# Performance work log

Hardware: AMD Instinct MI355X
Metric: run time of the kernel (lower is better)

Reference implementation:

```python
import jax, jax.numpy as jnp
import numpy as np
from jax import lax

G = 8      # deform groups (weight groups == offset groups)
K = 3      # kernel size
K2 = K * K


def conv3x3(x, w, b):
    # NCHW, 3x3, stride 1, padding 1 (SAME)
    y = lax.conv_general_dilated(x, w, (1, 1), 'SAME',
                                 dimension_numbers=('NCHW', 'OIHW', 'NCHW'))
    return y + b[None, :, None, None]


def deform_conv2d(ref, offsets, w, b):
    # ref: [B,C,H,W], offsets: [B,2*G*K2,H,W] (torchvision layout: per group,
    # per kernel position, (dy, dx) pairs), w: [C_out, C_in/G, K, K], b: [C_out]
    B, C, H, W = ref.shape
    Cg = C // G
    off = offsets.reshape(B, G, K2, 2, H, W)
    dy = off[:, :, :, 0]  # [B,G,K2,H,W]
    dx = off[:, :, :, 1]
    ky = (jnp.arange(K2) // K - K // 2).astype(ref.dtype)  # kernel y offsets (pad=1)
    kx = (jnp.arange(K2) % K - K // 2).astype(ref.dtype)
    base_y = jnp.arange(H, dtype=ref.dtype)[:, None] + ky[:, None, None]  # [K2,H,1]
    base_x = jnp.arange(W, dtype=ref.dtype)[None, :] + kx[:, None, None]  # [K2,1,W]
    py = dy + base_y  # [B,G,K2,H,W]
    px = dx + base_x

    y0 = jnp.floor(py).astype(jnp.int32)
    x0 = jnp.floor(px).astype(jnp.int32)
    ly = py - y0.astype(ref.dtype)
    lx = px - x0.astype(ref.dtype)

    ref_flat = ref.reshape(B, G, Cg, H * W)

    def gather(yi, xi):
        valid = (yi >= 0) & (yi < H) & (xi >= 0) & (xi < W)
        idx = jnp.clip(yi, 0, H - 1) * W + jnp.clip(xi, 0, W - 1)  # [B,G,K2,H,W]
        vals = jnp.take_along_axis(ref_flat, idx.reshape(B, G, 1, K2 * H * W), axis=3)
        vals = vals.reshape(B, G, Cg, K2, H, W)
        return vals * valid[:, :, None].astype(ref.dtype)

    w00 = ((1 - ly) * (1 - lx))[:, :, None]
    w01 = ((1 - ly) * lx)[:, :, None]
    w10 = (ly * (1 - lx))[:, :, None]
    w11 = (ly * lx)[:, :, None]
    sampled = (w00 * gather(y0, x0) + w01 * gather(y0, x0 + 1)
               + w10 * gather(y0 + 1, x0) + w11 * gather(y0 + 1, x0 + 1))
    # grouped accumulation: weight [C_out, Cg, K, K] -> [G, OCg, Cg, K2]
    wg = w.reshape(G, C // G, Cg, K2)
    out = jnp.einsum('bgikhw,goik->bgohw', sampled, wg)
    return out.reshape(B, C, H, W) + b[None, :, None, None]


def setup_inputs() -> dict:
    key = jax.random.key(0)
    ks = jax.random.split(key, 10)
    B, C, H, W = 2, 64, 256, 256
    s64 = 1.0 / np.sqrt(C * 9)
    s128 = 1.0 / np.sqrt(128 * 9)
    return {
        'offset': jax.random.normal(ks[0], (B, C, H, W), jnp.float32),
        'ref': jax.random.normal(ks[1], (B, C, H, W), jnp.float32),
        'w_off': jax.random.normal(ks[2], (2 * K2 * G, C, K, K), jnp.float32) * s64,
        'b_off': jnp.zeros((2 * K2 * G,), jnp.float32),
        'w_def': jax.random.normal(ks[3], (C, C // G, K, K), jnp.float32) * (1.0 / np.sqrt((C // G) * 9)),
        'b_def': jnp.zeros((C,), jnp.float32),
        'w_r1': jax.random.normal(ks[4], (C, 2 * C, K, K), jnp.float32) * s128,
        'b_r1': jnp.zeros((C,), jnp.float32),
        'w_r2': jax.random.normal(ks[5], (C, C, K, K), jnp.float32) * s64,
        'b_r2': jnp.zeros((C,), jnp.float32),
    }


def reference(offset, ref, w_off, b_off, w_def, b_def, w_r1, b_r1, w_r2, b_r2):
    deform_offsets = conv3x3(offset, w_off, b_off)              # [B,144,H,W]
    aligned_ref = deform_conv2d(ref, deform_offsets, w_def, b_def)
    x = jnp.concatenate([ref, aligned_ref], axis=1)             # [B,128,H,W]
    x = jax.nn.relu(conv3x3(x, w_r1, b_r1))
    x = jax.nn.relu(conv3x3(x, w_r2, b_r2))
    return x + aligned_ref
```

## Files before the change

### kernel.cpp

```cpp
#include <hip/hip_runtime.h>

typedef __attribute__((ext_vector_type(8)))  short  short8;
typedef __attribute__((ext_vector_type(4)))  float  float4v;
typedef __attribute__((ext_vector_type(16))) float  float16v;
typedef __attribute__((ext_vector_type(2)))  float  f32x2;

constexpr int HH = 256, WW = 256;
constexpr int PD = 258;
constexpr int PR = 260;
constexpr size_t HWsz = (size_t)HH * WW;

__device__ inline unsigned short f2bf(float f) {
    unsigned int u = __builtin_bit_cast(unsigned int, f);
    u += 0x7FFFu + ((u >> 16) & 1u);
    return (unsigned short)(u >> 16);
}
__device__ inline float bfhalf(unsigned int w, int hi) {
    return __builtin_bit_cast(float, hi ? (w & 0xFFFF0000u) : (w << 16));
}
__device__ inline f32x2 unpk2(unsigned int w) {
    f32x2 r;
    r.x = __builtin_bit_cast(float, w << 16);
    r.y = __builtin_bit_cast(float, w & 0xFFFF0000u);
    return r;
}
__device__ inline f32x2 splat2(float s) { f32x2 r; r.x = s; r.y = s; return r; }

template<int CDST, bool WRITE_G>
__global__ __launch_bounds__(256) void nchw_to_nhwc(
    const float* __restrict__ src, unsigned short* __restrict__ dst,
    unsigned short* __restrict__ dst_g)
{
    const int px = threadIdx.x, h = blockIdx.x, bi = blockIdx.y;
    const float* s = src + (size_t)bi * 64 * HWsz + (size_t)h * WW + px;
    unsigned short* d = dst + (((size_t)bi * PD + (h + 1)) * PD + (px + 1)) * CDST;
#pragma unroll
    for (int cg = 0; cg < 8; ++cg) {
        float v[8];
#pragma unroll
        for (int j = 0; j < 8; ++j) v[j] = s[(size_t)(cg * 8 + j) * HWsz];
        uint4 pk;
        pk.x = f2bf(v[0]) | ((unsigned)f2bf(v[1]) << 16);
        pk.y = f2bf(v[2]) | ((unsigned)f2bf(v[3]) << 16);
        pk.z = f2bf(v[4]) | ((unsigned)f2bf(v[5]) << 16);
        pk.w = f2bf(v[6]) | ((unsigned)f2bf(v[7]) << 16);
        *(uint4*)&d[cg * 8] = pk;
        if (WRITE_G) {
            unsigned short* dg = dst_g +
                ((size_t)(bi * 8 + cg) * PR * PR + (size_t)(h + 1) * PR + (px + 1)) * 8;
            *(uint4*)dg = pk;
        }
    }
}

__global__ __launch_bounds__(256) void zero_border(
    unsigned short* __restrict__ p_off, unsigned short* __restrict__ p_cat,
    unsigned short* __restrict__ p_x1, unsigned short* __restrict__ refg)
{
    const int bi = blockIdx.y, which = blockIdx.z;
    if (which == 3) {
        const int total = 8 * 1548;
        for (int i = blockIdx.x * 256 + threadIdx.x; i < total; i += gridDim.x * 256) {
            int g = i / 1548, t = i - g * 1548;
            int r, c;
            if (t < 780)  { int rr = t / 260; c = t - rr * 260; r = rr == 0 ? 0 : 256 + rr; }
            else          { int u = t - 780; int cc = u >> 8; r = 1 + (u & 255); c = cc == 0 ? 0 : 256 + cc; }
            uint4 z = {0, 0, 0, 0};
            *(uint4*)&refg[((size_t)(bi * 8 + g) * PR * PR + (size_t)r * PR + c) * 8] = z;
        }
        return;
    }
    unsigned short* buf = which == 0 ? p_off : (which == 1 ? p_cat : p_x1);
    const int CIN = (which == 1) ? 128 : 64;
    const int NG = CIN / 8;
    unsigned short* p = buf + (size_t)bi * PD * PD * CIN;
    const int total = 1028 * 16;
    for (int i = blockIdx.x * 256 + threadIdx.x; i < total; i += gridDim.x * 256) {
        int g = i & 15;
        if (g >= NG) continue;
        int pxi = i >> 4;
        int r, c;
        if (pxi < 258)       { r = 0;   c = pxi; }
        else if (pxi < 516)  { r = 257; c = pxi - 258; }
        else if (pxi < 772)  { r = pxi - 516 + 1; c = 0; }
        else                 { r = pxi - 772 + 1; c = 257; }
        uint4 z = {0, 0, 0, 0};
        *(uint4*)&p[((size_t)r * PD + c) * CIN + g * 8] = z;
    }
}

__device__ inline void pack_one(const float* __restrict__ w, short* __restrict__ wpk,
                                int Cout, int Cin, int e)
{
    int j = e & 7;
    int lane = (e >> 3) & 63;
    int ksp = 9 * (Cin / 16);
    int kstep = (e >> 9) % ksp;
    int cot = (e >> 9) / ksp;
    int tap = kstep / (Cin / 16);
    int ci = (kstep % (Cin / 16)) * 16 + (lane >> 5) * 8 + j;
    int co = cot * 32 + (lane & 31);
    float v = (co < Cout) ? w[((size_t)co * Cin + ci) * 9 + tap] : 0.f;
    wpk[e] = (short)f2bf(v);
}

__global__ __launch_bounds__(256) void pack_all(
    const float* __restrict__ w1, short* __restrict__ d1,
    const float* __restrict__ w2, short* __restrict__ d2,
    const float* __restrict__ w3, short* __restrict__ d3)
{
    int e = blockIdx.x * 256 + threadIdx.x;
    if (e < 110592)               pack_one(w1, d1, 144, 64, e);
    else if (e < 110592 + 73728)  pack_one(w2, d2, 64, 128, e - 110592);
    else if (e < 221184)          pack_one(w3, d3, 64, 64,  e - 184320);
}

template<int CIN, int COF, int COTB, int MODE, int MINW>
__global__ __launch_bounds__(256, MINW) void conv_mfma_nb(
    const unsigned short* __restrict__ src,
    const short* __restrict__ wpk,
    const float* __restrict__ bias,
    unsigned short* __restrict__ dst_bf,
    float* __restrict__ dst_f,
    const unsigned short* __restrict__ resid_bf)
{
    constexpr int CHUNKS = CIN / 32;
    constexpr int KST = 9 * (CIN / 16);
    constexpr int WSEG = 3 * 4 * 66 * 8;

    __shared__ unsigned short lds[4 * WSEG];

    const int tid  = threadIdx.x;
    const int lane = tid & 63;
    const int wv   = tid >> 6;
    const int half = lane >> 5;
    const int n32  = lane & 31;
    const int h  = blockIdx.x;
    const int bi = blockIdx.y / COTB;
    const int cb = blockIdx.y % COTB;
    const int cbase = cb * COF * 32;

    unsigned short* my = lds + wv * WSEG;
    const unsigned short* srcB = src + (size_t)bi * PD * PD * CIN;
    const short8* wbase = (const short8*)wpk;

    float16v acc[COF][2];
#pragma unroll
    for (int f = 0; f < COF; ++f) {
        float16v bv;
#pragma unroll
        for (int reg = 0; reg < 16; ++reg) {
            int co = cbase + f * 32 + (reg >> 2) * 8 + 4 * half + (reg & 3);
            float b = 0.f;
            if (MODE != 0 || co < 144) b = bias[co];
            bv[reg] = b;
        }
        acc[f][0] = bv;
        acc[f][1] = bv;
    }

    for (int ch = 0; ch < CHUNKS; ++ch) {
        const unsigned short* gband = srcB + ((size_t)h * PD + wv * 64) * CIN + ch * 32;
#pragma unroll
        for (int i0 = 0; i0 < 264; i0 += 64) {
            int i = i0 + lane;
            if (i0 + 64 > 264 && i >= 264) continue;
            int px = i >> 2, o = i & 3;
#pragma unroll
            for (int r = 0; r < 3; ++r) {
                uint4 v = *(const uint4*)(gband + ((size_t)r * PD + px) * CIN + o * 8);
                *(uint4*)&my[(((size_t)r * 4 + o) * 66 + px) * 8] = v;
            }
        }

#pragma unroll
        for (int tap = 0; tap < 9; ++tap) {
            const int row = tap / 3, dxo = tap % 3;
#pragma unroll
            for (int s = 0; s < 2; ++s) {
                const int kstep = tap * (CIN / 16) + ch * 2 + s;
                short8 a[COF];
#pragma unroll
                for (int f = 0; f < COF; ++f)
                    a[f] = wbase[((size_t)(cb * COF + f) * KST + kstep) * 64 + lane];
#pragma unroll
                for (int nt = 0; nt < 2; ++nt) {
                    short8 b = *(const short8*)
                        &my[(((size_t)row * 4 + s * 2 + half) * 66 + nt * 32 + dxo + n32) * 8];
#pragma unroll
                    for (int f = 0; f < COF; ++f)
                        acc[f][nt] = __builtin_amdgcn_mfma_f32_32x32x16_bf16(a[f], b, acc[f][nt], 0, 0, 0);
                }
            }
        }
    }

#pragma unroll
    for (int f = 0; f < COF; ++f) {
#pragma unroll
        for (int nt = 0; nt < 2; ++nt) {
            const int px = wv * 64 + nt * 32 + n32;
            float16v a = acc[f][nt];
#pragma unroll
            for (int q = 0; q < 4; ++q) {
                const int co4 = cbase + f * 32 + q * 8 + 4 * half;
                float v0 = a[q * 4 + 0], v1 = a[q * 4 + 1];
                float v2 = a[q * 4 + 2], v3 = a[q * 4 + 3];
                if (MODE == 0) {
                    if (co4 < 144) {
                        unsigned short* d = dst_bf + (size_t)bi * HWsz * 144;
                        uint2 pk;
                        pk.x = f2bf(v0) | ((unsigned)f2bf(v1) << 16);
                        pk.y = f2bf(v2) | ((unsigned)f2bf(v3) << 16);
                        *(uint2*)&d[((size_t)h * WW + px) * 144 + co4] = pk;
                    }
                } else if (MODE == 1) {
                    unsigned short* d = dst_bf + (size_t)bi * PD * PD * 64;
                    uint2 pk;
                    pk.x = f2bf(fmaxf(v0, 0.f)) | ((unsigned)f2bf(fmaxf(v1, 0.f)) << 16);
                    pk.y = f2bf(fmaxf(v2, 0.f)) | ((unsigned)f2bf(fmaxf(v3, 0.f)) << 16);
                    *(uint2*)&d[(((size_t)h + 1) * PD + (px + 1)) * 64 + co4] = pk;
                } else {
                    const unsigned short* rp = resid_bf + (size_t)bi * PD * PD * 128;
                    uint2 rv = *(const uint2*)&rp[(((size_t)h + 1) * PD + (px + 1)) * 128 + 64 + co4];
                    float r0 = bfhalf(rv.x, 0), r1 = bfhalf(rv.x, 1);
                    float r2 = bfhalf(rv.y, 0), r3 = bfhalf(rv.y, 1);
                    float* d = dst_f + (size_t)bi * 64 * HWsz + (size_t)h * WW + px;
                    d[(size_t)(co4 + 0) * HWsz] = fmaxf(v0, 0.f) + r0;
                    d[(size_t)(co4 + 1) * HWsz] = fmaxf(v1, 0.f) + r1;
                    d[(size_t)(co4 + 2) * HWsz] = fmaxf(v2, 0.f) + r2;
                    d[(size_t)(co4 + 3) * HWsz] = fmaxf(v3, 0.f) + r3;
                }
            }
        }
    }
}

__global__ __launch_bounds__(256) void deform_k7(
    const unsigned short* __restrict__ refg,
    const unsigned short* __restrict__ doff,
    const float* __restrict__ wdef, const float* __restrict__ bdef,
    unsigned short* __restrict__ pcat_out)
{
    __shared__ float wsm2[576];
    const int L = blockIdx.x;
    const int xcd = L & 7;
    const int j = L >> 3;
    const int g = j & 7;
    const int r = (j >> 3) & 31;
    const int bi = j >> 8;
    const int h = xcd * 32 + r;
    const int px = threadIdx.x;

    for (int i = threadIdx.x; i < 576; i += 256) {
        int o = i & 7, c = (i >> 3) & 7, k = i >> 6;
        wsm2[i] = wdef[(size_t)g * 576 + o * 72 + c * 9 + k];
    }
    __syncthreads();

    const unsigned int* dp = (const unsigned int*)(
        doff + (((size_t)bi * HWsz) + (size_t)h * WW + px) * 144 + g * 18);
    unsigned int dw[9];
#pragma unroll
    for (int k = 0; k < 9; ++k) dw[k] = dp[k];

    f32x2 acc2[4];
#pragma unroll
    for (int o = 0; o < 4; ++o) {
        acc2[o].x = bdef[g * 8 + 2 * o];
        acc2[o].y = bdef[g * 8 + 2 * o + 1];
    }

    const unsigned short* rb = refg + (size_t)(bi * 8 + g) * PR * PR * 8;
    const float hf = (float)h, pxf = (float)px;

#pragma unroll
    for (int k = 0; k < 9; ++k) {
        float dy = bfhalf(dw[k], 0);
        float dx = bfhalf(dw[k], 1);
        float py  = dy + (hf + (float)(k / 3 - 1));
        float pxs = dx + (pxf + (float)(k % 3 - 1));
        py  = fminf(fmaxf(py,  -1.f), 256.f);
        pxs = fminf(fmaxf(pxs, -1.f), 256.f);
        float fy = floorf(py), fx = floorf(pxs);
        float ly = py - fy, lx = pxs - fx;
        int y0 = (int)fy, x0 = (int)fx;
        int i00 = (y0 + 1) * PR + (x0 + 1);
        float omly = 1.f - ly, omlx = 1.f - lx;
        f32x2 w00 = splat2(omly * omlx), w01 = splat2(omly * lx);
        f32x2 w10 = splat2(ly * omlx),  w11 = splat2(ly * lx);

        const uint4 q00 = *(const uint4*)(rb + (size_t)i00 * 8);
        const uint4 q01 = *(const uint4*)(rb + (size_t)(i00 + 1) * 8);
        const uint4 q10 = *(const uint4*)(rb + (size_t)(i00 + PR) * 8);
        const uint4 q11 = *(const uint4*)(rb + (size_t)(i00 + PR + 1) * 8);
        union U { uint4 v; unsigned int a[4]; };
        U u00{q00}, u01{q01}, u10{q10}, u11{q11};

#pragma unroll
        for (int cw = 0; cw < 4; ++cw) {
            f32x2 sv = unpk2(u00.a[cw]) * w00;
            sv = __builtin_elementwise_fma(unpk2(u01.a[cw]), w01, sv);
            sv = __builtin_elementwise_fma(unpk2(u10.a[cw]), w10, sv);
            sv = __builtin_elementwise_fma(unpk2(u11.a[cw]), w11, sv);
            f32x2 bx = splat2(sv.x);
            f32x2 by = splat2(sv.y);
            const f32x2* wpa = (const f32x2*)&wsm2[((k * 8) + cw * 2) * 8];
            const f32x2* wpb = (const f32x2*)&wsm2[((k * 8) + cw * 2 + 1) * 8];
#pragma unroll
            for (int o = 0; o < 4; ++o) {
                acc2[o] = __builtin_elementwise_fma(wpa[o], bx, acc2[o]);
                acc2[o] = __builtin_elementwise_fma(wpb[o], by, acc2[o]);
            }
        }
    }

    unsigned short* po = pcat_out + (((size_t)bi * PD + (h + 1)) * PD + (px + 1)) * 128 + 64 + g * 8;
    uint4 pk;
    pk.x = f2bf(acc2[0].x) | ((unsigned)f2bf(acc2[0].y) << 16);
    pk.y = f2bf(acc2[1].x) | ((unsigned)f2bf(acc2[1].y) << 16);
    pk.z = f2bf(acc2[2].x) | ((unsigned)f2bf(acc2[2].y) << 16);
    pk.w = f2bf(acc2[3].x) | ((unsigned)f2bf(acc2[3].y) << 16);
    *(uint4*)po = pk;
}

extern "C" void kernel_launch(void* const* d_in, const int* in_sizes, int n_in,
                              void* d_out, int out_size, void* d_ws, size_t ws_size,
                              hipStream_t stream)
{
    const float* offset = (const float*)d_in[0];
    const float* ref    = (const float*)d_in[1];
    const float* w_off  = (const float*)d_in[2];
    const float* b_off  = (const float*)d_in[3];
    const float* w_def  = (const float*)d_in[4];
    const float* b_def  = (const float*)d_in[5];
    const float* w_r1   = (const float*)d_in[6];
    const float* b_r1   = (const float*)d_in[7];
    const float* w_r2   = (const float*)d_in[8];
    const float* b_r2   = (const float*)d_in[9];
    float* out = (float*)d_out;

    unsigned short* p_off = (unsigned short*)d_ws;
    unsigned short* p_cat = p_off + (size_t)8520192;
    unsigned short* p_x1  = p_cat + (size_t)17040384;
    unsigned short* doff  = p_x1 + (size_t)8520192;
    unsigned short* refg  = doff + (size_t)18874368;
    short* wpk1  = (short*)(refg + (size_t)8652800);
    short* wpkr1 = wpk1 + 110592;
    short* wpkr2 = wpkr1 + 73728;

    zero_border<<<dim3(65, 2, 4), 256, 0, stream>>>(p_off, p_cat, p_x1, refg);

    pack_all<<<dim3((221184 + 255) / 256), 256, 0, stream>>>(
        w_off, wpk1, w_r1, wpkr1, w_r2, wpkr2);

    nchw_to_nhwc<64, false><<<dim3(256, 2), 256, 0, stream>>>(offset, p_off, nullptr);
    nchw_to_nhwc<128, true><<<dim3(256, 2), 256, 0, stream>>>(ref, p_cat, refg);

    conv_mfma_nb<64, 2, 3, 0, 3><<<dim3(256, 6), 256, 0, stream>>>(
        p_off, wpk1, b_off, doff, nullptr, nullptr);

    deform_k7<<<dim3(4096), 256, 0, stream>>>(refg, doff, w_def, b_def, p_cat);

    conv_mfma_nb<128, 2, 1, 1, 3><<<dim3(256, 2), 256, 0, stream>>>(
        p_cat, wpkr1, b_r1, p_x1, nullptr, nullptr);

    conv_mfma_nb<64, 2, 1, 2, 3><<<dim3(256, 2), 256, 0, stream>>>(
        p_x1, wpkr2, b_r2, nullptr, out, p_cat);
}
```

Before: 336.4 us.

## Double-buffer deform gathers and read prepacked weights from global instead of LDS

The deformable conv kernel now issues the four bilinear gathers for the next tap before doing the arithmetic for the current tap, using two register buffers to hide gather latency. The deform weights are repacked once in pack_all into a per-group float layout in workspace, so the kernel reads them through uniform global loads. This removes the per-block LDS fill and __syncthreads. A launch bound of 6 blocks per SM is also added. The extra live registers for the second buffer may limit occupancy, and scalar or global weight reads may be slower than LDS broadcast.

Result: slower. 478.0 us (+42.1%).

```diff
diff --git a/kernel.cpp b/kernel.cpp
--- a/kernel.cpp
+++ b/kernel.cpp
@@ -107,12 +107,19 @@
 __global__ __launch_bounds__(256) void pack_all(
     const float* __restrict__ w1, short* __restrict__ d1,
     const float* __restrict__ w2, short* __restrict__ d2,
-    const float* __restrict__ w3, short* __restrict__ d3)
+    const float* __restrict__ w3, short* __restrict__ d3,
+    const float* __restrict__ wdef, float* __restrict__ wdefp)
 {
     int e = blockIdx.x * 256 + threadIdx.x;
     if (e < 110592)               pack_one(w1, d1, 144, 64, e);
     else if (e < 110592 + 73728)  pack_one(w2, d2, 64, 128, e - 110592);
     else if (e < 221184)          pack_one(w3, d3, 64, 64,  e - 184320);
+    else if (e < 221184 + 4608) {
+        int t = e - 221184;
+        int o = t & 7, c = (t >> 3) & 7, gk = t >> 6;
+        int g = gk / 9, k = gk - g * 9;
+        wdefp[t] = wdef[(size_t)g * 576 + o * 72 + c * 9 + k];
+    }
 }
 
 template<int CIN, int COF, int COTB, int MODE, int MINW>
@@ -236,13 +243,63 @@
     }
 }
 
-__global__ __launch_bounds__(256) void deform_k7(
+__device__ __forceinline__ void tap_setup(int k, const unsigned int* dw,
+    float hf, float pxf, int& i00, float& ly, float& lx)
+{
+    float dy = bfhalf(dw[k], 0);
+    float dx = bfhalf(dw[k], 1);
+    float py  = dy + (hf + (float)(k / 3 - 1));
+    float pxs = dx + (pxf + (float)(k % 3 - 1));
+    py  = fminf(fmaxf(py,  -1.f), 256.f);
+    pxs = fminf(fmaxf(pxs, -1.f), 256.f);
+    float fy = floorf(py), fx = floorf(pxs);
+    ly = py - fy; lx = pxs - fx;
+    i00 = ((int)fy + 1) * PR + ((int)fx + 1);
+}
+
+__device__ __forceinline__ void tap_load(const unsigned short* __restrict__ rb,
+                                         int i00, uint4* q)
+{
+    q[0] = *(const uint4*)(rb + (size_t)(unsigned)i00 * 8);
+    q[1] = *(const uint4*)(rb + (size_t)(unsigned)(i00 + 1) * 8);
+    q[2] = *(const uint4*)(rb + (size_t)(unsigned)(i00 + PR) * 8);
+    q[3] = *(const uint4*)(rb + (size_t)(unsigned)(i00 + PR + 1) * 8);
+}
+
+__device__ __forceinline__ void tap_consume(const uint4* q, float ly, float lx,
+    const float* __restrict__ wq, f32x2* acc2)
+{
+    float omly = 1.f - ly, omlx = 1.f - lx;
+    f32x2 W00 = splat2(omly * omlx), W01 = splat2(omly * lx);
+    f32x2 W10 = splat2(ly * omlx),  W11 = splat2(ly * lx);
+    const unsigned int* a00 = (const unsigned int*)&q[0];
+    const unsigned int* a01 = (const unsigned int*)&q[1];
+    const unsigned int* a10 = (const unsigned int*)&q[2];
+    const unsigned int* a11 = (const unsigned int*)&q[3];
+#pragma unroll
+    for (int cw = 0; cw < 4; ++cw) {
+        f32x2 s = unpk2(a00[cw]) * W00;
+        s = __builtin_elementwise_fma(unpk2(a01[cw]), W01, s);
+        s = __builtin_elementwise_fma(unpk2(a10[cw]), W10, s);
+        s = __builtin_elementwise_fma(unpk2(a11[cw]), W11, s);
+        f32x2 bx; bx.x = s.x; bx.y = s.x;
+        f32x2 by; by.x = s.y; by.y = s.y;
+        const f32x2* wpa = (const f32x2*)(wq + (cw * 2) * 8);
+        const f32x2* wpb = (const f32x2*)(wq + (cw * 2 + 1) * 8);
+#pragma unroll
+        for (int o = 0; o < 4; ++o) {
+            acc2[o] = __builtin_elementwise_fma(wpa[o], bx, acc2[o]);
+            acc2[o] = __builtin_elementwise_fma(wpb[o], by, acc2[o]);
+        }
+    }
+}
+
+__global__ __launch_bounds__(256, 6) void deform_k8(
     const unsigned short* __restrict__ refg,
     const unsigned short* __restrict__ doff,
-    const float* __restrict__ wdef, const float* __restrict__ bdef,
+    const float* __restrict__ wdefp, const float* __restrict__ bdef,
     unsigned short* __restrict__ pcat_out)
 {
-    __shared__ float wsm2[576];
     const int L = blockIdx.x;
     const int xcd = L & 7;
     const int j = L >> 3;
@@ -252,12 +309,6 @@
     const int h = xcd * 32 + r;
     const int px = threadIdx.x;
 
-    for (int i = threadIdx.x; i < 576; i += 256) {
-        int o = i & 7, c = (i >> 3) & 7, k = i >> 6;
-        wsm2[i] = wdef[(size_t)g * 576 + o * 72 + c * 9 + k];
-    }
-    __syncthreads();
-
     const unsigned int* dp = (const unsigned int*)(
         doff + (((size_t)bi * HWsz) + (size_t)h * WW + px) * 144 + g * 18);
     unsigned int dw[9];
@@ -272,47 +323,21 @@
     }
 
     const unsigned short* rb = refg + (size_t)(bi * 8 + g) * PR * PR * 8;
+    const float* wg = wdefp + (size_t)g * 9 * 64;
     const float hf = (float)h, pxf = (float)px;
 
+    uint4 qa[4], qb[4];
+    int i00; float lyc, lxc, lyn = 0.f, lxn = 0.f;
+    tap_setup(0, dw, hf, pxf, i00, lyc, lxc);
+    tap_load(rb, i00, qa);
 #pragma unroll
     for (int k = 0; k < 9; ++k) {
-        float dy = bfhalf(dw[k], 0);
-        float dx = bfhalf(dw[k], 1);
-        float py  = dy + (hf + (float)(k / 3 - 1));
-        float pxs = dx + (pxf + (float)(k % 3 - 1));
-        py  = fminf(fmaxf(py,  -1.f), 256.f);
-        pxs = fminf(fmaxf(pxs, -1.f), 256.f);
-        float fy = floorf(py), fx = floorf(pxs);
-        float ly = py - fy, lx = pxs - fx;
-        int y0 = (int)fy, x0 = (int)fx;
-        int i00 = (y0 + 1) * PR + (x0 + 1);
-        float omly = 1.f - ly, omlx = 1.f - lx;
-        f32x2 w00 = splat2(omly * omlx), w01 = splat2(omly * lx);
-        f32x2 w10 = splat2(ly * omlx),  w11 = splat2(ly * lx);
-
-        const uint4 q00 = *(const uint4*)(rb + (size_t)i00 * 8);
-        const uint4 q01 = *(const uint4*)(rb + (size_t)(i00 + 1) * 8);
-        const uint4 q10 = *(const uint4*)(rb + (size_t)(i00 + PR) * 8);
-        const uint4 q11 = *(const uint4*)(rb + (size_t)(i00 + PR + 1) * 8);
-        union U { uint4 v; unsigned int a[4]; };
-        U u00{q00}, u01{q01}, u10{q10}, u11{q11};
-
-#pragma unroll
-        for (int cw = 0; cw < 4; ++cw) {
-            f32x2 sv = unpk2(u00.a[cw]) * w00;
-            sv = __builtin_elementwise_fma(unpk2(u01.a[cw]), w01, sv);
-            sv = __builtin_elementwise_fma(unpk2(u10.a[cw]), w10, sv);
-            sv = __builtin_elementwise_fma(unpk2(u11.a[cw]), w11, sv);
-            f32x2 bx = splat2(sv.x);
-            f32x2 by = splat2(sv.y);
-            const f32x2* wpa = (const f32x2*)&wsm2[((k * 8) + cw * 2) * 8];
-            const f32x2* wpb = (const f32x2*)&wsm2[((k * 8) + cw * 2 + 1) * 8];
-#pragma unroll
-            for (int o = 0; o < 4; ++o) {
-                acc2[o] = __builtin_elementwise_fma(wpa[o], bx, acc2[o]);
-                acc2[o] = __builtin_elementwise_fma(wpb[o], by, acc2[o]);
-            }
-        }
+        if (k < 8) {
+            tap_setup(k + 1, dw, hf, pxf, i00, lyn, lxn);
+            tap_load(rb, i00, (k & 1) ? qa : qb);
+        }
+        tap_consume((k & 1) ? qb : qa, lyc, lxc, wg + k * 64, acc2);
+        lyc = lyn; lxc = lxn;
     }
 
     unsigned short* po = pcat_out + (((size_t)bi * PD + (h + 1)) * PD + (px + 1)) * 128 + 64 + g * 8;
@@ -348,11 +373,12 @@
     short* wpk1  = (short*)(refg + (size_t)8652800);
     short* wpkr1 = wpk1 + 110592;
     short* wpkr2 = wpkr1 + 73728;
+    float* wdefp = (float*)(wpkr2 + 36864);
 
     zero_border<<<dim3(65, 2, 4), 256, 0, stream>>>(p_off, p_cat, p_x1, refg);
 
-    pack_all<<<dim3((221184 + 255) / 256), 256, 0, stream>>>(
-        w_off, wpk1, w_r1, wpkr1, w_r2, wpkr2);
+    pack_all<<<dim3((225792 + 255) / 256), 256, 0, stream>>>(
+        w_off, wpk1, w_r1, wpkr1, w_r2, wpkr2, w_def, wdefp);
 
     nchw_to_nhwc<64, false><<<dim3(256, 2), 256, 0, stream>>>(offset, p_off, nullptr);
     nchw_to_nhwc<128, true><<<dim3(256, 2), 256, 0, stream>>>(ref, p_cat, refg);
@@ -360,7 +386,7 @@
     conv_mfma_nb<64, 2, 3, 0, 3><<<dim3(256, 6), 256, 0, stream>>>(
         p_off, wpk1, b_off, doff, nullptr, nullptr);
 
-    deform_k7<<<dim3(4096), 256, 0, stream>>>(refg, doff, w_def, b_def, p_cat);
+    deform_k8<<<dim3(4096), 256, 0, stream>>>(refg, doff, wdefp, b_def, p_cat);
 
     conv_mfma_nb<128, 2, 1, 1, 3><<<dim3(256, 2), 256, 0, stream>>>(
         p_cat, wpkr1, b_r1, p_x1, nullptr, nullptr);
```
